# Kernel tuning notes

Measured on AMD Instinct MI355X. Metric: run time of the kernel, lower is better.

## Reference

```python
import jax, jax.numpy as jnp
import numpy as np

E = 1024  # embed_dim
H = 1     # num_heads (energy_W matmul forces head_dim == embed_dim)
TEMPERATURE = 1.0


def setup_inputs() -> dict:
    key = jax.random.key(0)
    ks = jax.random.split(key, 10)
    B, S = 8, 2048
    inp = {
        "query": jax.random.normal(ks[0], (B, S, E), dtype=jnp.float32),
        "key": jax.random.normal(ks[1], (B, S, E), dtype=jnp.float32),
        "value": jax.random.normal(ks[2], (B, S, E), dtype=jnp.float32),
        "mask": jnp.ones((1, 1, S, S), dtype=jnp.int32),
        # nn.Linear params (y = x @ W.T + b)
        "Wq": jax.random.normal(ks[3], (E, E), dtype=jnp.float32) * (1.0 / np.sqrt(E)),
        "bq": jnp.zeros((E,), dtype=jnp.float32),
        "Wk": jax.random.normal(ks[4], (E, E), dtype=jnp.float32) * (1.0 / np.sqrt(E)),
        "bk": jnp.zeros((E,), dtype=jnp.float32),
        "Wv": jax.random.normal(ks[5], (E, E), dtype=jnp.float32) * (1.0 / np.sqrt(E)),
        "bv": jnp.zeros((E,), dtype=jnp.float32),
        "energy_W": jax.random.normal(ks[6], (E, E), dtype=jnp.float32),
    }
    return inp


def reference(query, key, value, mask, Wq, bq, Wk, bk, Wv, bv, energy_W):
    B, S, _ = query.shape
    hd = E // H
    # projections (torch Linear: x @ W.T + b), then split heads -> [B, H, S, hd]
    q = (query @ Wq.T + bq).reshape(B, S, H, hd).transpose(0, 2, 1, 3)
    k = (key @ Wk.T + bk).reshape(B, S, H, hd).transpose(0, 2, 1, 3)
    v = (value @ Wv.T + bv).reshape(B, S, H, hd).transpose(0, 2, 1, 3)
    # bilinear energy: (q) @ (k @ W)^T   -> [B, H, Sq, Sk]
    k_t = k @ energy_W
    energy = jnp.einsum("bhqd,bhkd->bhqk", q, k_t) / TEMPERATURE
    energy = jnp.where(mask == 0, jnp.float32(-1e9), energy)
    attn_weights = jax.nn.softmax(-energy, axis=-1)
    out = jnp.einsum("bhqk,bhkd->bhqd", attn_weights, v)
    out = out.transpose(0, 2, 1, 3).reshape(B, S, E)
    return (out, attn_weights)
```

## Files before the change

kernel.cpp:

```cpp
#include <hip/hip_runtime.h>


typedef __attribute__((ext_vector_type(8))) short short8;
typedef __attribute__((ext_vector_type(4))) float f32x4;

#define E_DIM 1024
#define S_LEN 2048
#define NB 8

__device__ __forceinline__ unsigned short rne_bf(float x) {
    unsigned int u = __float_as_uint(x);
    return (unsigned short)((u + 0x7fffu + ((u >> 16) & 1u)) >> 16);
}

__device__ __forceinline__ void splitbf(float x, unsigned short& h, unsigned short& l) {
    unsigned int u = __float_as_uint(x);
    unsigned int rh = ((u + 0x7fffu + ((u >> 16) & 1u)) >> 16) << 16;
    h = (unsigned short)(rh >> 16);
    float r = x - __uint_as_float(rh);
    unsigned int v = __float_as_uint(r);
    l = (unsigned short)((v + 0x7fffu + ((v >> 16) & 1u)) >> 16);
}

__device__ __forceinline__ void lds_cp16(const void* g, void* l) {
    __builtin_amdgcn_global_load_lds(
        (const __attribute__((address_space(1))) unsigned int*)g,
        (__attribute__((address_space(3))) unsigned int*)l, 16, 0, 0);
}

__device__ __forceinline__ void wait_vm4() { asm volatile("s_waitcnt vmcnt(4)" ::: "memory"); }
__device__ __forceinline__ void wait_vm3() { asm volatile("s_waitcnt vmcnt(3)" ::: "memory"); }
__device__ __forceinline__ void wait_vm0() { asm volatile("s_waitcnt vmcnt(0)" ::: "memory"); }

__device__ __forceinline__ void swizzle_xy(int& bx, int& by) {
    const int gx = gridDim.x, gy = gridDim.y;
    const int nwg = gx * gy;
    const int w = by * gx + bx;
    if ((gx & 3) == 0 && (gy & 3) == 0 && (((gx >> 2) * (gy >> 2)) & 7) == 0) {
        const int nchx = gx >> 2;
        const int xcd = w & 7, i = w >> 3;
        const int j = i >> 4, p = i & 15;
        const int ch = xcd + 8 * j;
        const int chy = ch / nchx, chx = ch - chy * nchx;
        by = chy * 4 + (p >> 2);
        bx = chx * 4 + (p & 3);
    } else if ((nwg & 7) == 0) {
        const int cpx = nwg >> 3;
        const int sw = (w & 7) * cpx + (w >> 3);
        bx = sw % gx;
        by = sw / gx;
    }
}

template <bool DO_L>
__global__ __launch_bounds__(256) void conv_img(
    const float* __restrict__ src, unsigned short* __restrict__ h,
    unsigned short* __restrict__ l, int ld, int nkt)
{
    const int t = threadIdx.x;
    const long long tb = ((long long)blockIdx.y * nkt + blockIdx.x) * 4096;
    const float* s0 = src + (long long)blockIdx.y * 128 * ld + blockIdx.x * 32;
#pragma unroll
    for (int i = 0; i < 4; ++i) {
        const int f = i * 256 + t;
        const int r = f >> 3;
        const int c4 = (f & 7) << 2;
        const float4 v = *(const float4*)(s0 + (long long)r * ld + c4);
        const int gg = c4 >> 3;
        const int half = (c4 >> 2) & 1;
        const long long wo = tb + (long long)(gg * 128 + r) * 8 + half * 4;
        unsigned short h0, h1, h2, h3;
        if (DO_L) {
            unsigned short l0, l1, l2, l3;
            splitbf(v.x, h0, l0); splitbf(v.y, h1, l1);
            splitbf(v.z, h2, l2); splitbf(v.w, h3, l3);
            uint2 hp, lp;
            hp.x = h0 | ((unsigned)h1 << 16); hp.y = h2 | ((unsigned)h3 << 16);
            lp.x = l0 | ((unsigned)l1 << 16); lp.y = l2 | ((unsigned)l3 << 16);
            *(uint2*)(h + wo) = hp;
            *(uint2*)(l + wo) = lp;
        } else {
            h0 = rne_bf(v.x); h1 = rne_bf(v.y); h2 = rne_bf(v.z); h3 = rne_bf(v.w);
            uint2 hp;
            hp.x = h0 | ((unsigned)h1 << 16); hp.y = h2 | ((unsigned)h3 << 16);
            *(uint2*)(h + wo) = hp;
        }
    }
}

__global__ __launch_bounds__(256) void conv_imgT(
    const float* __restrict__ src, unsigned short* __restrict__ h,
    unsigned short* __restrict__ l, int nkt)
{
    __shared__ float tile[32][132];
    const int t = threadIdx.x;
    const int kt = blockIdx.x;
    const int rb = blockIdx.y;
    const float* s0 = src + (long long)kt * 32 * E_DIM + rb * 128;
#pragma unroll
    for (int i = 0; i < 4; ++i) {
        const int f = i * 256 + t;
        const int r = f >> 5;
        const int c4 = (f & 31) << 2;
        const float4 v = *(const float4*)(s0 + (long long)r * E_DIM + c4);
        tile[r][c4] = v.x; tile[r][c4 + 1] = v.y;
        tile[r][c4 + 2] = v.z; tile[r][c4 + 3] = v.w;
    }
    __syncthreads();
    const long long tb = ((long long)rb * nkt + kt) * 4096;
#pragma unroll
    for (int i = 0; i < 2; ++i) {
        const int c = i * 256 + t;
        const int g = c >> 7, r = c & 127;
        unsigned short hh[8], ll[8];
#pragma unroll
        for (int j = 0; j < 8; ++j) splitbf(tile[g * 8 + j][r], hh[j], ll[j]);
        uint4 hp, lp;
        hp.x = hh[0] | ((unsigned)hh[1] << 16); hp.y = hh[2] | ((unsigned)hh[3] << 16);
        hp.z = hh[4] | ((unsigned)hh[5] << 16); hp.w = hh[6] | ((unsigned)hh[7] << 16);
        lp.x = ll[0] | ((unsigned)ll[1] << 16); lp.y = ll[2] | ((unsigned)ll[3] << 16);
        lp.z = ll[4] | ((unsigned)ll[5] << 16); lp.w = ll[6] | ((unsigned)ll[7] << 16);
        *(uint4*)(h + tb + (long long)c * 8) = hp;
        *(uint4*)(l + tb + (long long)c * 8) = lp;
    }
}

template <int NPROD>
__global__ __launch_bounds__(512, 4) void gemm_big(
    const unsigned short* __restrict__ Ah, const unsigned short* __restrict__ Al,
    const unsigned short* __restrict__ Bh, const unsigned short* __restrict__ Bl,
    float* __restrict__ C, const float* __restrict__ bias,
    int ldC, long long bsC, int nkt, int aZrb, int bZrb)
{
    __shared__ unsigned short smb[36864];

    const int t = threadIdx.x;
    const int wv = t >> 6, lane = t & 63;
    const int wr = wv >> 1, wc = wv & 1;
    const int lr = lane & 15, gq = lane >> 4;

    int bx = blockIdx.x, by = blockIdx.y;
    swizzle_xy(bx, by);

    const long long aB0 = ((long long)blockIdx.z * aZrb + 2 * by) * nkt * 4096;
    const long long aB1 = aB0 + (long long)nkt * 4096;
    const long long bB0 = ((long long)blockIdx.z * bZrb + bx) * nkt * 4096;

    auto srcptr = [&](int s, const unsigned short*& a0, const unsigned short*& a1,
                      const unsigned short*& bS) {
        int seg, kt;
        if (NPROD == 3) {
            seg = (s >= 2 * nkt) ? 2 : (s >= nkt ? 1 : 0);
            kt = s - seg * nkt;
        } else { seg = 0; kt = s; }
        const unsigned short* aBase = ((NPROD == 3 && seg == 1) ? Al : Ah);
        const unsigned short* bBase = ((NPROD == 3 && seg == 2) ? Bl : Bh);
        a0 = aBase + aB0 + (long long)kt * 4096;
        a1 = aBase + aB1 + (long long)kt * 4096;
        bS = bBase + bB0 + (long long)kt * 4096;
    };
    auto stage = [&](const unsigned short* a0, const unsigned short* a1,
                     const unsigned short* bS, int c) {
        unsigned short* dA = smb + c * 12288;
        lds_cp16(a0 + t * 8, dA + t * 8);
        lds_cp16(a1 + t * 8, dA + 4096 + t * 8);
        lds_cp16(bS + t * 8, dA + 8192 + t * 8);
    };

    short8 af[4], bfr[4];
    auto loadFrags = [&](int c) {
        const unsigned short* dA = smb + c * 12288;
        const unsigned short* dB = dA + 8192;
#pragma unroll
        for (int m = 0; m < 4; ++m) {
            const int R = wr * 64 + m * 16 + lr;
            af[m] = *(const short8*)(dA + (R >> 7) * 4096 + (gq * 128 + (R & 127)) * 8);
        }
#pragma unroll
        for (int n = 0; n < 4; ++n) {
            const int Cc = wc * 64 + n * 16 + lr;
            bfr[n] = *(const short8*)(dB + (gq * 128 + Cc) * 8);
        }
    };

    f32x4 acc[4][4] = {};
    const int nsteps = NPROD * nkt;

    {
        const unsigned short *a0, *a1, *bS;
        srcptr(0, a0, a1, bS); stage(a0, a1, bS, 0);
        srcptr(1, a0, a1, bS); stage(a0, a1, bS, 1);
    }
    wait_vm3();
    __builtin_amdgcn_s_barrier();
    __builtin_amdgcn_sched_barrier(0);
    loadFrags(0);

    for (int s = 0; s < nsteps; ++s) {
        if (s + 2 < nsteps) {
            const unsigned short *a0, *a1, *bS;
            srcptr(s + 2, a0, a1, bS);
            stage(a0, a1, bS, (s + 2) % 3);
        }
        __builtin_amdgcn_sched_barrier(0);
        __builtin_amdgcn_s_setprio(1);
#pragma unroll
        for (int m = 0; m < 4; ++m)
#pragma unroll
            for (int n = 0; n < 4; ++n)
                acc[m][n] = __builtin_amdgcn_mfma_f32_16x16x32_bf16(af[m], bfr[n], acc[m][n], 0, 0, 0);
        __builtin_amdgcn_s_setprio(0);
        __builtin_amdgcn_sched_barrier(0);
        if (s + 1 < nsteps) {
            if (s + 2 < nsteps) wait_vm3();
            else wait_vm0();
            __builtin_amdgcn_s_barrier();
            __builtin_amdgcn_sched_barrier(0);
            loadFrags((s + 1) % 3);
        }
    }

    const int cr = (lane >> 4) << 2, cc = lane & 15;
    float* Cb = C + (long long)blockIdx.z * bsC;
#pragma unroll
    for (int m = 0; m < 4; ++m)
#pragma unroll
        for (int n = 0; n < 4; ++n) {
            const int gc = bx * 128 + wc * 64 + n * 16 + cc;
            const float badd = bias ? bias[gc] : 0.0f;
            const int gr0 = by * 256 + wr * 64 + m * 16 + cr;
#pragma unroll
            for (int i = 0; i < 4; ++i)
                Cb[(long long)(gr0 + i) * ldC + gc] = acc[m][n][i] + badd;
        }
}

template <int NPROD, int WMODE>
__global__ __launch_bounds__(256) void gemm_img(
    const unsigned short* __restrict__ Ah, const unsigned short* __restrict__ Al,
    const unsigned short* __restrict__ Bh, const unsigned short* __restrict__ Bl,
    float* __restrict__ C, const float* __restrict__ bias,
    unsigned short* __restrict__ imgH, unsigned short* __restrict__ imgL,
    int ldC, long long bsC, int nkt, int aZrb, int bZrb, int outNkt)
{
    extern __shared__ unsigned short sm[];

    const int t = threadIdx.x;
    const int wv = t >> 6, lane = t & 63;
    const int wm = (wv >> 1) << 6, wn = (wv & 1) << 6;
    const int lr = lane & 15, gq = lane >> 4;

    int bx = blockIdx.x, by = blockIdx.y;
    swizzle_xy(bx, by);

    const long long aB0 = ((long long)blockIdx.z * aZrb + by) * nkt * 4096;
    const long long bB0 = ((long long)blockIdx.z * bZrb + bx) * nkt * 4096;

    auto srcptr = [&](int s, const unsigned short*& aS, const unsigned short*& bS) {
        int seg, kt;
        if (NPROD == 3) {
            seg = (s >= 2 * nkt) ? 2 : (s >= nkt ? 1 : 0);
            kt = s - seg * nkt;
        } else { seg = 0; kt = s; }
        aS = ((NPROD == 3 && seg == 1) ? Al : Ah) + aB0 + (long long)kt * 4096;
        bS = ((NPROD == 3 && seg == 2) ? Bl : Bh) + bB0 + (long long)kt * 4096;
    };
    auto stage = [&](const unsigned short* aS, const unsigned short* bS, int c) {
        unsigned short* dA = sm + c * 8192;
        unsigned short* dB = dA + 4096;
#pragma unroll
        for (int j = 0; j < 2; ++j) {
            lds_cp16(aS + (wv * 128 + j * 64 + lane) * 8, dA + (wv * 128 + j * 64) * 8);
            lds_cp16(bS + (wv * 128 + j * 64 + lane) * 8, dB + (wv * 128 + j * 64) * 8);
        }
    };

    short8 af[4], bfr[4];
    auto loadFrags = [&](int c) {
        const unsigned short* smA = sm + c * 8192;
        const unsigned short* smB = smA + 4096;
        const unsigned short* pa = smA + (gq * 128 + wm + lr) * 8;
        const unsigned short* pb = smB + (gq * 128 + wn + lr) * 8;
#pragma unroll
        for (int m = 0; m < 4; ++m) af[m] = *(const short8*)(pa + m * 128);
#pragma unroll
        for (int n = 0; n < 4; ++n) bfr[n] = *(const short8*)(pb + n * 128);
    };

    f32x4 acc[4][4] = {};
    const int nsteps = NPROD * nkt;

    {
        const unsigned short *aS, *bS;
        srcptr(0, aS, bS); stage(aS, bS, 0);
        srcptr(1, aS, bS); stage(aS, bS, 1);
    }
    wait_vm4();
    __builtin_amdgcn_s_barrier();
    __builtin_amdgcn_sched_barrier(0);
    loadFrags(0);

    for (int s = 0; s < nsteps; ++s) {
        if (s + 2 < nsteps) {
            const unsigned short *aS, *bS;
            srcptr(s + 2, aS, bS);
            stage(aS, bS, (s + 2) % 3);
        }
        __builtin_amdgcn_sched_barrier(0);
        __builtin_amdgcn_s_setprio(1);
#pragma unroll
        for (int m = 0; m < 4; ++m)
#pragma unroll
            for (int n = 0; n < 4; ++n)
                acc[m][n] = __builtin_amdgcn_mfma_f32_16x16x32_bf16(af[m], bfr[n], acc[m][n], 0, 0, 0);
        __builtin_amdgcn_s_setprio(0);
        __builtin_amdgcn_sched_barrier(0);
        if (s + 1 < nsteps) {
            if (s + 2 < nsteps) wait_vm4();
            else wait_vm0();
            __builtin_amdgcn_s_barrier();
            __builtin_amdgcn_sched_barrier(0);
            loadFrags((s + 1) % 3);
        }
    }

    const int cr = (lane >> 4) << 2, cc = lane & 15;
    if (WMODE == 0) {
        float* Cb = C + (long long)blockIdx.z * bsC;
#pragma unroll
        for (int m = 0; m < 4; ++m)
#pragma unroll
            for (int n = 0; n < 4; ++n) {
                const int gc = bx * 128 + wn + n * 16 + cc;
                const float badd = bias ? bias[gc] : 0.0f;
                const int gr0 = by * 128 + wm + m * 16 + cr;
#pragma unroll
                for (int i = 0; i < 4; ++i)
                    Cb[(long long)(gr0 + i) * ldC + gc] = acc[m][n][i] + badd;
            }
    } else {
        float* slab = (float*)sm;
        const int wmi = wv >> 1;
#pragma unroll
        for (int m = 0; m < 4; ++m) {
            __syncthreads();
#pragma unroll
            for (int n = 0; n < 4; ++n) {
                const int col = wn + n * 16 + cc;
                const float badd = bias ? bias[bx * 128 + col] : 0.0f;
#pragma unroll
                for (int i = 0; i < 4; ++i)
                    slab[(wmi * 16 + cr + i) * 132 + col] = acc[m][n][i] + badd;
            }
            __syncthreads();
            if (WMODE == 1) {
#pragma unroll
                for (int it = 0; it < 2; ++it) {
                    const int e = it * 256 + t;
                    const int wq = e >> 8, cg = (e >> 4) & 15, fr = e & 15;
                    const float* sp = slab + (wq * 16 + fr) * 132 + cg * 8;
                    const int rIn = wq * 64 + m * 16 + fr;
                    const int ktO = bx * 4 + (cg >> 2);
                    const int gO = cg & 3;
                    const long long base =
                        ((long long)by * outNkt + ktO) * 4096 + (gO * 128 + rIn) * 8;
                    unsigned short h[8], l[8];
#pragma unroll
                    for (int j = 0; j < 8; ++j) splitbf(sp[j], h[j], l[j]);
                    uint4 hp, lp;
                    hp.x = h[0] | ((unsigned)h[1] << 16); hp.y = h[2] | ((unsigned)h[3] << 16);
                    hp.z = h[4] | ((unsigned)h[5] << 16); hp.w = h[6] | ((unsigned)h[7] << 16);
                    lp.x = l[0] | ((unsigned)l[1] << 16); lp.y = l[2] | ((unsigned)l[3] << 16);
                    lp.z = l[4] | ((unsigned)l[5] << 16); lp.w = l[6] | ((unsigned)l[7] << 16);
                    *(uint4*)(imgH + base) = hp;
                    *(uint4*)(imgL + base) = lp;
                }
            } else {
#pragma unroll
                for (int it = 0; it < 2; ++it) {
                    const int e = it * 256 + t;
                    const int wq = e >> 8, s8 = (e >> 7) & 1, dl = e & 127;
                    const int sG = by * 128 + wq * 64 + m * 16 + s8 * 8;
                    const int z = sG >> 11, sIn = sG & 2047;
                    const int ktO = sIn >> 5, gO = (sIn >> 3) & 3;
                    const long long base =
                        ((long long)(z * 8 + bx) * 64 + ktO) * 4096 + (gO * 128 + dl) * 8;
                    unsigned short h[8];
#pragma unroll
                    for (int j = 0; j < 8; ++j)
                        h[j] = rne_bf(slab[(wq * 16 + s8 * 8 + j) * 132 + dl]);
                    uint4 hp;
                    hp.x = h[0] | ((unsigned)h[1] << 16); hp.y = h[2] | ((unsigned)h[3] << 16);
                    hp.z = h[4] | ((unsigned)h[5] << 16); hp.w = h[6] | ((unsigned)h[7] << 16);
                    *(uint4*)(imgH + base) = hp;
                }
            }
        }
    }
}

__global__ __launch_bounds__(256) void softmax_img(
    float* __restrict__ attn, const int* __restrict__ mask,
    unsigned short* __restrict__ img)
{
    const int row = blockIdx.x;
    const int q = row & (S_LEN - 1);
    const int t = threadIdx.x;
    const int lane = t & 63, wid = t >> 6;
    float* rp = attn + (long long)row * S_LEN;
    const int* mp = mask + (long long)q * S_LEN;

    const float4 e0 = *(const float4*)(rp + t * 8);
    const float4 e1 = *(const float4*)(rp + t * 8 + 4);
    const int4 ma = *(const int4*)(mp + t * 8);
    const int4 mb = *(const int4*)(mp + t * 8 + 4);
    float zv[8];
    zv[0] = ma.x ? -e0.x : 1e9f;
    zv[1] = ma.y ? -e0.y : 1e9f;
    zv[2] = ma.z ? -e0.z : 1e9f;
    zv[3] = ma.w ? -e0.w : 1e9f;
    zv[4] = mb.x ? -e1.x : 1e9f;
    zv[5] = mb.y ? -e1.y : 1e9f;
    zv[6] = mb.z ? -e1.z : 1e9f;
    zv[7] = mb.w ? -e1.w : 1e9f;
    float mx = zv[0];
#pragma unroll
    for (int j = 1; j < 8; ++j) mx = fmaxf(mx, zv[j]);
#pragma unroll
    for (int o = 32; o > 0; o >>= 1) mx = fmaxf(mx, __shfl_xor(mx, o));
    __shared__ float redm[4], reds[4];
    if (lane == 0) redm[wid] = mx;
    __syncthreads();
    mx = fmaxf(fmaxf(redm[0], redm[1]), fmaxf(redm[2], redm[3]));
    float s = 0.f;
#pragma unroll
    for (int j = 0; j < 8; ++j) { zv[j] = expf(zv[j] - mx); s += zv[j]; }
#pragma unroll
    for (int o = 32; o > 0; o >>= 1) s += __shfl_xor(s, o);
    if (lane == 0) reds[wid] = s;
    __syncthreads();
    s = reds[0] + reds[1] + reds[2] + reds[3];
    const float inv = 1.0f / s;
    float4 o0, o1;
    o0.x = zv[0] * inv; o0.y = zv[1] * inv; o0.z = zv[2] * inv; o0.w = zv[3] * inv;
    o1.x = zv[4] * inv; o1.y = zv[5] * inv; o1.z = zv[6] * inv; o1.w = zv[7] * inv;
    *(float4*)(rp + t * 8) = o0;
    *(float4*)(rp + t * 8 + 4) = o1;
    const int z = row >> 11, rb = (row >> 7) & 15;
    const int ktO = t >> 2, gO = t & 3, r = row & 127;
    const long long base = (((long long)(z * 16 + rb) * 64 + ktO) * 512 + gO * 128 + r) * 8;
    uint4 hp;
    hp.x = rne_bf(o0.x) | ((unsigned)rne_bf(o0.y) << 16);
    hp.y = rne_bf(o0.z) | ((unsigned)rne_bf(o0.w) << 16);
    hp.z = rne_bf(o1.x) | ((unsigned)rne_bf(o1.y) << 16);
    hp.w = rne_bf(o1.z) | ((unsigned)rne_bf(o1.w) << 16);
    *(uint4*)(img + base) = hp;
}

__global__ void transpose1024(const float* __restrict__ in, float* __restrict__ out)
{
    __shared__ float tile[32][33];
    const int bx = blockIdx.x << 5, by = blockIdx.y << 5;
    const int tx = threadIdx.x, ty = threadIdx.y;
#pragma unroll
    for (int i = 0; i < 4; ++i)
        tile[ty + 8 * i][tx] = in[(long long)(by + ty + 8 * i) * E_DIM + bx + tx];
    __syncthreads();
#pragma unroll
    for (int i = 0; i < 4; ++i)
        out[(long long)(bx + ty + 8 * i) * E_DIM + by + tx] = tile[tx][ty + 8 * i];
}

__global__ __launch_bounds__(256) void bias_c_kernel(
    const float* __restrict__ We, const float* __restrict__ bq, float* __restrict__ c)
{
    const int i = blockIdx.x;
    const int t = threadIdx.x;
    float s = 0.f;
    for (int d = t; d < E_DIM; d += 256) s += bq[d] * We[(long long)i * E_DIM + d];
#pragma unroll
    for (int o = 32; o > 0; o >>= 1) s += __shfl_xor(s, o);
    __shared__ float red[4];
    if ((t & 63) == 0) red[t >> 6] = s;
    __syncthreads();
    if (t == 0) c[i] = red[0] + red[1] + red[2] + red[3];
}

template <bool SPLIT, int WMODE>
__global__ __launch_bounds__(256) void gemm_split(
    const float* __restrict__ A, const float* __restrict__ B,
    float* __restrict__ C, const float* __restrict__ bias,
    int M, int N, int K,
    long long bsA, long long bsB, long long bsC)
{
    extern __shared__ unsigned short sm[];
    unsigned short* sAh = sm;
    unsigned short* sBh = sm + 5120;
    unsigned short* sAl = sm + 10240;
    unsigned short* sBl = sm + 15360;

    const int t = threadIdx.x;
    const int z = blockIdx.z;
    const float* Ab = A + (long long)z * bsA + (long long)blockIdx.y * 128 * K;
    const float* Bb = B + (long long)z * bsB + (long long)blockIdx.x * 128 * K;

    const int wv = t >> 6;
    const int lane = t & 63;
    const int wm = (wv >> 1) << 6;
    const int wn = (wv & 1) << 6;
    const int lr = lane & 15;
    const int ko = (lane >> 4) << 3;

    f32x4 acc[4][4] = {};

    for (int k0 = 0; k0 < K; k0 += 32) {
        __syncthreads();
#pragma unroll
        for (int i = 0; i < 4; ++i) {
            const int f = t + (i << 8);
            const int row = f >> 3;
            const int c4 = (f & 7) << 2;
            const float4 av = *(const float4*)(Ab + (long long)row * K + k0 + c4);
            const float4 bv = *(const float4*)(Bb + (long long)row * K + k0 + c4);
            if (SPLIT) {
                unsigned short h0, h1, h2, h3, l0, l1, l2, l3;
                splitbf(av.x, h0, l0); splitbf(av.y, h1, l1);
                splitbf(av.z, h2, l2); splitbf(av.w, h3, l3);
                uint2 hp, lp;
                hp.x = (unsigned)h0 | ((unsigned)h1 << 16);
                hp.y = (unsigned)h2 | ((unsigned)h3 << 16);
                lp.x = (unsigned)l0 | ((unsigned)l1 << 16);
                lp.y = (unsigned)l2 | ((unsigned)l3 << 16);
                *(uint2*)(sAh + row * 40 + c4) = hp;
                *(uint2*)(sAl + row * 40 + c4) = lp;
                splitbf(bv.x, h0, l0); splitbf(bv.y, h1, l1);
                splitbf(bv.z, h2, l2); splitbf(bv.w, h3, l3);
                hp.x = (unsigned)h0 | ((unsigned)h1 << 16);
                hp.y = (unsigned)h2 | ((unsigned)h3 << 16);
                lp.x = (unsigned)l0 | ((unsigned)l1 << 16);
                lp.y = (unsigned)l2 | ((unsigned)l3 << 16);
                *(uint2*)(sBh + row * 40 + c4) = hp;
                *(uint2*)(sBl + row * 40 + c4) = lp;
            } else {
                uint2 hp;
                hp.x = (unsigned)rne_bf(av.x) | ((unsigned)rne_bf(av.y) << 16);
                hp.y = (unsigned)rne_bf(av.z) | ((unsigned)rne_bf(av.w) << 16);
                *(uint2*)(sAh + row * 40 + c4) = hp;
                hp.x = (unsigned)rne_bf(bv.x) | ((unsigned)rne_bf(bv.y) << 16);
                hp.y = (unsigned)rne_bf(bv.z) | ((unsigned)rne_bf(bv.w) << 16);
                *(uint2*)(sBh + row * 40 + c4) = hp;
            }
        }
        __syncthreads();
        short8 ah[4], bh[4], al[4], bl[4];
#pragma unroll
        for (int m = 0; m < 4; ++m)
            ah[m] = *(const short8*)(sAh + (wm + m * 16 + lr) * 40 + ko);
#pragma unroll
        for (int n = 0; n < 4; ++n)
            bh[n] = *(const short8*)(sBh + (wn + n * 16 + lr) * 40 + ko);
        if (SPLIT) {
#pragma unroll
            for (int m = 0; m < 4; ++m)
                al[m] = *(const short8*)(sAl + (wm + m * 16 + lr) * 40 + ko);
#pragma unroll
            for (int n = 0; n < 4; ++n)
                bl[n] = *(const short8*)(sBl + (wn + n * 16 + lr) * 40 + ko);
        }
#pragma unroll
        for (int m = 0; m < 4; ++m) {
#pragma unroll
            for (int n = 0; n < 4; ++n) {
                acc[m][n] = __builtin_amdgcn_mfma_f32_16x16x32_bf16(ah[m], bh[n], acc[m][n], 0, 0, 0);
                if (SPLIT) {
                    acc[m][n] = __builtin_amdgcn_mfma_f32_16x16x32_bf16(ah[m], bl[n], acc[m][n], 0, 0, 0);
                    acc[m][n] = __builtin_amdgcn_mfma_f32_16x16x32_bf16(al[m], bh[n], acc[m][n], 0, 0, 0);
                }
            }
        }
    }

    const int cr = (lane >> 4) << 2;
    const int cc = lane & 15;
    float* Cb = C + (long long)z * bsC;
#pragma unroll
    for (int m = 0; m < 4; ++m) {
#pragma unroll
        for (int n = 0; n < 4; ++n) {
            const int gc = blockIdx.x * 128 + wn + n * 16 + cc;
            const float badd = bias ? bias[gc] : 0.0f;
            const int gr0 = blockIdx.y * 128 + wm + m * 16 + cr;
#pragma unroll
            for (int i = 0; i < 4; ++i) {
                const float val = acc[m][n][i] + badd;
                if (WMODE == 0) {
                    Cb[(long long)(gr0 + i) * N + gc] = val;
                } else {
                    const int r = gr0 + i;
                    Cb[(long long)(r >> 11) * ((long long)N * 2048) +
                       (long long)gc * 2048 + (r & 2047)] = val;
                }
            }
        }
    }
}

__global__ __launch_bounds__(256) void softmax_rows(
    float* __restrict__ attn, const int* __restrict__ mask)
{
    const int row = blockIdx.x;
    const int q = row & (S_LEN - 1);
    const int t = threadIdx.x;
    const int lane = t & 63, wid = t >> 6;
    float* rp = attn + (long long)row * S_LEN;
    const int* mp = mask + (long long)q * S_LEN;

    float zv[8];
    float mx = -3.4e38f;
#pragma unroll
    for (int j = 0; j < 8; ++j) {
        const int idx = t + (j << 8);
        const float e = rp[idx];
        const int mv = mp[idx];
        const float zz = (mv != 0) ? -e : 1e9f;
        zv[j] = zz;
        mx = fmaxf(mx, zz);
    }
#pragma unroll
    for (int o = 32; o > 0; o >>= 1) mx = fmaxf(mx, __shfl_xor(mx, o));
    __shared__ float redm[4], reds[4];
    if (lane == 0) redm[wid] = mx;
    __syncthreads();
    mx = fmaxf(fmaxf(redm[0], redm[1]), fmaxf(redm[2], redm[3]));

    float s = 0.f;
#pragma unroll
    for (int j = 0; j < 8; ++j) { zv[j] = expf(zv[j] - mx); s += zv[j]; }
#pragma unroll
    for (int o = 32; o > 0; o >>= 1) s += __shfl_xor(s, o);
    if (lane == 0) reds[wid] = s;
    __syncthreads();
    s = reds[0] + reds[1] + reds[2] + reds[3];
    const float inv = 1.0f / s;
#pragma unroll
    for (int j = 0; j < 8; ++j) rp[t + (j << 8)] = zv[j] * inv;
}

extern "C" void kernel_launch(void* const* d_in, const int* in_sizes, int n_in,
                              void* d_out, int out_size, void* d_ws, size_t ws_size,
                              hipStream_t stream)
{
    const float* query = (const float*)d_in[0];
    const float* key   = (const float*)d_in[1];
    const float* value = (const float*)d_in[2];
    const int*   mask  = (const int*)d_in[3];
    const float* Wq    = (const float*)d_in[4];
    const float* bq    = (const float*)d_in[5];
    const float* Wk    = (const float*)d_in[6];
    const float* bk    = (const float*)d_in[7];
    const float* Wv    = (const float*)d_in[8];
    const float* bv    = (const float*)d_in[9];
    const float* We    = (const float*)d_in[10];

    float* out  = (float*)d_out;
    float* attn = out + (long long)NB * S_LEN * E_DIM;

    const size_t oWqT  = 0;
    const size_t oCvec = oWqT + (4u << 20);
    const size_t oWqTH = oCvec + 4096;
    const size_t oWqTL = oWqTH + (2u << 20);
    const size_t oWeH  = oWqTL + (2u << 20);
    const size_t oWeL  = oWeH + (2u << 20);
    const size_t oWkH  = oWeL + (2u << 20);
    const size_t oWkL  = oWkH + (2u << 20);
    const size_t oWvH  = oWkL + (2u << 20);
    const size_t oPH   = oWvH + (2u << 20);
    const size_t oPL   = oPH + (2u << 20);
    const size_t oBig1 = oPL + (2u << 20);
    const size_t oBig2 = oBig1 + (64u << 20);
    const size_t oBig3 = oBig2 + (64u << 20);
    const size_t NEED  = oBig3 + (64u << 20);

    char* wsb = (char*)d_ws;

    if (ws_size >= NEED) {
        float* cvec = (float*)(wsb + oCvec);
        unsigned short* WqTH = (unsigned short*)(wsb + oWqTH);
        unsigned short* WqTL = (unsigned short*)(wsb + oWqTL);
        unsigned short* WeH  = (unsigned short*)(wsb + oWeH);
        unsigned short* WeL  = (unsigned short*)(wsb + oWeL);
        unsigned short* WkH  = (unsigned short*)(wsb + oWkH);
        unsigned short* WkL  = (unsigned short*)(wsb + oWkL);
        unsigned short* WvH  = (unsigned short*)(wsb + oWvH);
        unsigned short* PH   = (unsigned short*)(wsb + oPH);
        unsigned short* PL   = (unsigned short*)(wsb + oPL);
        unsigned short* qryH = (unsigned short*)(wsb + oBig1);
        unsigned short* qryL = (unsigned short*)(wsb + oBig1 + (32u << 20));
        unsigned short* attnH = (unsigned short*)(wsb + oBig1);
        unsigned short* keyH = (unsigned short*)(wsb + oBig2);
        unsigned short* keyL = (unsigned short*)(wsb + oBig2 + (32u << 20));
        unsigned short* qwH  = (unsigned short*)(wsb + oBig2);
        unsigned short* qwL  = (unsigned short*)(wsb + oBig2 + (32u << 20));
        unsigned short* kH   = (unsigned short*)(wsb + oBig3);
        unsigned short* kL   = (unsigned short*)(wsb + oBig3 + (32u << 20));
        unsigned short* vTH  = (unsigned short*)(wsb + oBig3);
        unsigned short* valH = (unsigned short*)(wsb + oBig3 + (32u << 20));

        bias_c_kernel<<<1024, 256, 0, stream>>>(We, bq, cvec);
        conv_imgT<<<dim3(32, 8), 256, 0, stream>>>(Wq, WqTH, WqTL, 32);
        conv_img<true><<<dim3(32, 8), 256, 0, stream>>>(We, WeH, WeL, 1024, 32);
        conv_img<true><<<dim3(32, 8), 256, 0, stream>>>(Wk, WkH, WkL, 1024, 32);
        conv_img<false><<<dim3(32, 8), 256, 0, stream>>>(Wv, WvH, nullptr, 1024, 32);
        conv_img<true><<<dim3(32, 128), 256, 0, stream>>>(query, qryH, qryL, 1024, 32);
        conv_img<true><<<dim3(32, 128), 256, 0, stream>>>(key, keyH, keyL, 1024, 32);

        gemm_img<3, 1><<<dim3(8, 8, 1), 256, 49152, stream>>>(
            WeH, WeL, WqTH, WqTL, nullptr, nullptr, PH, PL, 0, 0, 32, 0, 0, 32);
        gemm_img<3, 1><<<dim3(8, 128, 1), 256, 49152, stream>>>(
            keyH, keyL, WkH, WkL, nullptr, bk, kH, kL, 0, 0, 32, 0, 0, 32);
        gemm_img<3, 1><<<dim3(8, 128, 1), 256, 49152, stream>>>(
            qryH, qryL, PH, PL, nullptr, cvec, qwH, qwL, 0, 0, 32, 0, 0, 32);
        gemm_big<3><<<dim3(16, 8, NB), 512, 0, stream>>>(
            qwH, qwL, kH, kL, attn, nullptr,
            2048, (long long)S_LEN * S_LEN, 32, 16, 16);
        conv_img<false><<<dim3(32, 128), 256, 0, stream>>>(value, valH, nullptr, 1024, 32);
        gemm_img<1, 3><<<dim3(8, 128, 1), 256, 49152, stream>>>(
            valH, nullptr, WvH, nullptr, nullptr, bv, vTH, nullptr, 0, 0, 32, 0, 0, 0);
        softmax_img<<<NB * S_LEN, 256, 0, stream>>>(attn, mask, attnH);
        gemm_big<1><<<dim3(8, 8, NB), 512, 0, stream>>>(
            attnH, nullptr, vTH, nullptr, out, nullptr,
            1024, (long long)S_LEN * E_DIM, 64, 16, 8);
    } else {
        float* ws   = (float*)d_ws;
        float* WqT  = ws;
        float* P    = WqT + 1048576;
        float* cvec = P + 1048576;
        float* kbuf = cvec + 1024;
        float* qw   = kbuf + 16777216;
        float* vT   = qw + 16777216;
        const size_t need_old = (size_t)(1048576 * 2 + 1024 + 16777216 * 3) * 4;
        if (ws_size < need_old) return;

        transpose1024<<<dim3(32, 32), dim3(32, 8), 0, stream>>>(Wq, WqT);
        bias_c_kernel<<<1024, 256, 0, stream>>>(We, bq, cvec);
        gemm_split<true, 0><<<dim3(8, 8, 1), 256, 40960, stream>>>(
            We, WqT, P, nullptr, 1024, 1024, 1024, 0, 0, 0);
        gemm_split<true, 0><<<dim3(8, 128, 1), 256, 40960, stream>>>(
            key, Wk, kbuf, bk, 16384, 1024, 1024, 0, 0, 0);
        gemm_split<false, 1><<<dim3(8, 128, 1), 256, 20480, stream>>>(
            value, Wv, vT, bv, 16384, 1024, 1024, 0, 0, 0);
        gemm_split<true, 0><<<dim3(8, 128, 1), 256, 40960, stream>>>(
            query, P, qw, cvec, 16384, 1024, 1024, 0, 0, 0);
        gemm_split<true, 0><<<dim3(16, 16, NB), 256, 40960, stream>>>(
            qw, kbuf, attn, nullptr, 2048, 2048, 1024,
            (long long)S_LEN * E_DIM, (long long)S_LEN * E_DIM, (long long)S_LEN * S_LEN);
        softmax_rows<<<NB * S_LEN, 256, 0, stream>>>(attn, mask);
        gemm_split<false, 0><<<dim3(8, 16, NB), 256, 20480, stream>>>(
            attn, vT, out, nullptr, 2048, 1024, 2048,
            (long long)S_LEN * S_LEN, (long long)E_DIM * S_LEN, (long long)S_LEN * E_DIM);
    }

    (void)in_sizes; (void)n_in; (void)out_size;
}
```

Measured before the change: 803.0 us.

## Add 32x32x16 MFMA kernel for split-bf16 energy GEMM with triple buffering

Adds a dedicated kernel for the energy GEMM (qw @ k^T) that uses 32x32x16 bf16 MFMA instructions in place of the generic gemm_big<3>. It stages tiles of 16 k-elements into a three-deep LDS ring using global_load_lds, with vmcnt waits and barriers, and raises wave priority around the MFMA block. The aim is fewer LDS fragment reads per FLOP and better overlap of loads with the three-product (hh, lh, hl) split-precision accumulation. The output is written directly as row-strided float stores from the 32x32 accumulator layout, which may be less coalesced than before.

```diff
diff --git a/kernel.cpp b/kernel.cpp
--- a/kernel.cpp
+++ b/kernel.cpp
@@ -3,6 +3,7 @@
 
 typedef __attribute__((ext_vector_type(8))) short short8;
 typedef __attribute__((ext_vector_type(4))) float f32x4;
+typedef __attribute__((ext_vector_type(16))) float f32x16;
 
 #define E_DIM 1024
 #define S_LEN 2048
@@ -28,6 +29,7 @@
         (__attribute__((address_space(3))) unsigned int*)l, 16, 0, 0);
 }
 
+__device__ __forceinline__ void wait_vm6() { asm volatile("s_waitcnt vmcnt(6)" ::: "memory"); }
 __device__ __forceinline__ void wait_vm4() { asm volatile("s_waitcnt vmcnt(4)" ::: "memory"); }
 __device__ __forceinline__ void wait_vm3() { asm volatile("s_waitcnt vmcnt(3)" ::: "memory"); }
 __device__ __forceinline__ void wait_vm0() { asm volatile("s_waitcnt vmcnt(0)" ::: "memory"); }
@@ -123,6 +125,110 @@
         *(uint4*)(h + tb + (long long)c * 8) = hp;
         *(uint4*)(l + tb + (long long)c * 8) = lp;
     }
+}
+
+__global__ __launch_bounds__(512, 4) void gemm_e3(
+    const unsigned short* __restrict__ Ah, const unsigned short* __restrict__ Al,
+    const unsigned short* __restrict__ Bh, const unsigned short* __restrict__ Bl,
+    float* __restrict__ C, int ldC, long long bsC, int nkt32, int aZrb, int bZrb)
+{
+    __shared__ unsigned short smb[36864];
+
+    const int t = threadIdx.x;
+    const int wv = t >> 6, lane = t & 63;
+    const int wr = wv >> 1, wc = wv & 1;
+    const int l31 = lane & 31, lh = lane >> 5;
+
+    int bx = blockIdx.x, by = blockIdx.y;
+    swizzle_xy(bx, by);
+
+    const long long aB0 = ((long long)blockIdx.z * aZrb + 2 * by) * nkt32 * 4096;
+    const long long aB1 = aB0 + (long long)nkt32 * 4096;
+    const long long bB0 = ((long long)blockIdx.z * bZrb + bx) * nkt32 * 4096;
+
+    const int rA = t & 255, glA = t >> 8;
+    const int bc = t & 255;
+    auto stage = [&](int k16, int c) {
+        unsigned short* buf = smb + c * 12288;
+        const int kt32 = k16 >> 1, hh = k16 & 1;
+        const long long aOff = ((rA >> 7) ? aB1 : aB0) + (long long)kt32 * 4096
+                             + ((2 * hh + glA) * 128 + (rA & 127)) * 8;
+        lds_cp16(Ah + aOff, buf + t * 8);
+        lds_cp16(Al + aOff, buf + 4096 + t * 8);
+        const long long bOff = bB0 + (long long)kt32 * 4096
+                             + ((2 * hh + (bc >> 7)) * 128 + (bc & 127)) * 8;
+        const unsigned short* bsrc = (t < 256) ? Bh : Bl;
+        lds_cp16(bsrc + bOff, buf + 8192 + t * 8);
+    };
+
+    short8 ah[2], al[2], bh[2], bl[2];
+    auto loadFrags = [&](int c) {
+        const unsigned short* buf = smb + c * 12288;
+#pragma unroll
+        for (int m = 0; m < 2; ++m) {
+            const int ra = lh * 256 + wr * 64 + m * 32 + l31;
+            ah[m] = *(const short8*)(buf + ra * 8);
+            al[m] = *(const short8*)(buf + 4096 + ra * 8);
+        }
+#pragma unroll
+        for (int n = 0; n < 2; ++n) {
+            const int rb = lh * 128 + wc * 64 + n * 32 + l31;
+            bh[n] = *(const short8*)(buf + 8192 + rb * 8);
+            bl[n] = *(const short8*)(buf + 10240 + rb * 8);
+        }
+    };
+
+    f32x16 acc[2][2] = {};
+    const int n16 = nkt32 * 2;
+
+    stage(0, 0);
+    stage(1, 1);
+
+    for (int s = 0; s < n16; ++s) {
+        __builtin_amdgcn_s_barrier();
+        if (s + 2 < n16) {
+            stage(s + 2, (s + 2) % 3);
+            wait_vm6();
+        } else if (s + 1 < n16) {
+            wait_vm3();
+        } else {
+            wait_vm0();
+        }
+        __builtin_amdgcn_s_barrier();
+        __builtin_amdgcn_sched_barrier(0);
+        loadFrags(s % 3);
+        __builtin_amdgcn_s_setprio(1);
+#pragma unroll
+        for (int m = 0; m < 2; ++m)
+#pragma unroll
+            for (int n = 0; n < 2; ++n)
+                acc[m][n] = __builtin_amdgcn_mfma_f32_32x32x16_bf16(ah[m], bh[n], acc[m][n], 0, 0, 0);
+#pragma unroll
+        for (int m = 0; m < 2; ++m)
+#pragma unroll
+            for (int n = 0; n < 2; ++n)
+                acc[m][n] = __builtin_amdgcn_mfma_f32_32x32x16_bf16(al[m], bh[n], acc[m][n], 0, 0, 0);
+#pragma unroll
+        for (int m = 0; m < 2; ++m)
+#pragma unroll
+            for (int n = 0; n < 2; ++n)
+                acc[m][n] = __builtin_amdgcn_mfma_f32_32x32x16_bf16(ah[m], bl[n], acc[m][n], 0, 0, 0);
+        __builtin_amdgcn_s_setprio(0);
+    }
+
+    float* Cb = C + (long long)blockIdx.z * bsC;
+#pragma unroll
+    for (int m = 0; m < 2; ++m)
+#pragma unroll
+        for (int n = 0; n < 2; ++n) {
+            const int gc = bx * 128 + wc * 64 + n * 32 + l31;
+            const int gr0 = by * 256 + wr * 64 + m * 32 + 4 * lh;
+#pragma unroll
+            for (int reg = 0; reg < 16; ++reg) {
+                const int row = (reg & 3) + 8 * (reg >> 2);
+                Cb[(long long)(gr0 + row) * ldC + gc] = acc[m][n][reg];
+            }
+        }
 }
 
 template <int NPROD>
@@ -720,8 +826,8 @@
             keyH, keyL, WkH, WkL, nullptr, bk, kH, kL, 0, 0, 32, 0, 0, 32);
         gemm_img<3, 1><<<dim3(8, 128, 1), 256, 49152, stream>>>(
             qryH, qryL, PH, PL, nullptr, cvec, qwH, qwL, 0, 0, 32, 0, 0, 32);
-        gemm_big<3><<<dim3(16, 8, NB), 512, 0, stream>>>(
-            qwH, qwL, kH, kL, attn, nullptr,
+        gemm_e3<<<dim3(16, 8, NB), 512, 0, stream>>>(
+            qwH, qwL, kH, kL, attn,
             2048, (long long)S_LEN * S_LEN, 32, 16, 16);
         conv_img<false><<<dim3(32, 128), 256, 0, stream>>>(value, valH, nullptr, 1024, 32);
         gemm_img<1, 3><<<dim3(8, 128, 1), 256, 49152, stream>>>(
```

Result: no change. 792.6 us (median of 2 runs) (-1.3%).
